# Kernel tuning notes

Measured on AMD Instinct MI355X. Metric: run time of the kernel, lower is better.

The kernel has to match this reference:

```python
import jax, jax.numpy as jnp
import numpy as np

EMB = 768
HEADS = 12
DH = EMB // HEADS


def setup_inputs() -> dict:
    key = jax.random.key(0)
    k = jax.random.split(key, 5)
    s = 0.02
    return {
        "x": jax.random.normal(k[0], (4, 2048, EMB), dtype=jnp.float32),
        "qkv_w": jax.random.normal(k[1], (3 * EMB, EMB), dtype=jnp.float32) * s,  # torch Linear weight [out,in]
        "qkv_b": jax.random.normal(k[2], (3 * EMB,), dtype=jnp.float32) * s,
        "proj_w": jax.random.normal(k[3], (EMB, EMB), dtype=jnp.float32) * s,
        "proj_b": jax.random.normal(k[4], (EMB,), dtype=jnp.float32) * s,
    }


def reference(x, qkv_w, qkv_b, proj_w, proj_b):
    b, n, _ = x.shape
    qkv = x @ qkv_w.T + qkv_b  # [b, n, 3*EMB]
    # rearrange 'b n (h d qkv) -> qkv b h n d'
    qkv = qkv.reshape(b, n, HEADS, DH, 3)
    qkv = jnp.transpose(qkv, (4, 0, 2, 1, 3))  # [3, b, h, n, d]
    q, k, v = qkv[0], qkv[1], qkv[2]
    e = jnp.einsum("bhqd,bhkd->bhqk", q, k)
    scale = jnp.float32(EMB) ** 0.5
    # NOTE: original divides by sqrt(emb_size) AFTER softmax (faithful to source)
    attn = jax.nn.softmax(e, axis=-1) / scale
    out = jnp.einsum("bhqk,bhkd->bhqd", attn, v)
    out = jnp.transpose(out, (0, 2, 1, 3)).reshape(b, n, EMB)  # 'b h n d -> b n (h d)'
    return out @ proj_w.T + proj_b
```

## Files before the change

### kernel.cpp

```cpp
#include <hip/hip_runtime.h>
#include <hip/hip_bf16.h>

typedef unsigned short ushort_t;
typedef __attribute__((ext_vector_type(8))) short s16x8;
typedef __attribute__((ext_vector_type(4))) float f32x4;
typedef __attribute__((ext_vector_type(16))) float f32x16;
typedef __attribute__((ext_vector_type(4))) unsigned int u32x4;

#define EMB 768
#define HEADS 12
#define DH 64
#define BATCH 4
#define SEQ 2048
#define MTOK (BATCH*SEQ)
#define NQKV (3*EMB)
#define LOG2E 1.44269504088896f

__device__ __forceinline__ ushort_t f2bf(float f) {
  unsigned u = __float_as_uint(f);
  u += 0x7fffu + ((u >> 16) & 1u);
  return (ushort_t)(u >> 16);
}
__device__ __forceinline__ unsigned pk2bf(float a, float b) {
  return (unsigned)f2bf(a) | ((unsigned)f2bf(b) << 16);
}
__device__ __forceinline__ unsigned cvtpk(float lo, float hi_) {
  unsigned d;
  asm("v_cvt_pk_bf16_f32 %0, %1, %2" : "=v"(d) : "v"(lo), "v"(hi_));
  return d;
}

__device__ __forceinline__ void gload_lds16(const void* g, void* l) {
  __builtin_amdgcn_global_load_lds(
      (const __attribute__((address_space(1))) unsigned*)g,
      (__attribute__((address_space(3))) unsigned*)l, 16, 0, 0);
}

__global__ void cvt_bf16(const float* __restrict__ in, ushort_t* __restrict__ out, int n4) {
  int i = blockIdx.x * blockDim.x + threadIdx.x;
  if (i >= n4) return;
  const float4 v = reinterpret_cast<const float4*>(in)[i];
  reinterpret_cast<uint2*>(out)[i] = make_uint2(pk2bf(v.x, v.y), pk2bf(v.z, v.w));
}

__global__ void cvt_wqkv(const float* __restrict__ w, const float* __restrict__ bias,
                         ushort_t* __restrict__ out, float* __restrict__ bias_p, int n4) {
  int i = blockIdx.x * blockDim.x + threadIdx.x;
  if (i >= n4) return;
  const int srcrow = i / 192;
  const int c4 = i - srcrow * 192;
  const int h = srcrow / 192;
  const int rem = srcrow - h * 192;
  const int d = rem / 3;
  const int which = rem - d * 3;
  const int dstrow = which * 768 + h * 64 + d;
  const float4 v = reinterpret_cast<const float4*>(w)[i];
  reinterpret_cast<uint2*>(out)[dstrow * 192 + c4] =
      make_uint2(pk2bf(v.x, v.y), pk2bf(v.z, v.w));
  if (c4 == 0) bias_p[dstrow] = bias[srcrow];
}

#define TM 128
#define TN 128
#define BKG 64
#define GSTEPS 12

template<int MODE>
__global__ __launch_bounds__(256, 2) void gemm_bt(
    const ushort_t* __restrict__ A, const ushort_t* __restrict__ BT,
    const float* __restrict__ bias, float* __restrict__ Cf,
    ushort_t* __restrict__ Qd, ushort_t* __restrict__ Kd, ushort_t* __restrict__ Vt,
    int M, int N, int K)
{
  __shared__ alignas(16) ushort_t As[2][TM*BKG];
  __shared__ alignas(16) ushort_t Bs[2][TN*BKG];
  const int t = threadIdx.x;
  const int w = t >> 6, l = t & 63, g = l >> 4, r = l & 15;
  const int wr = w >> 1, wc = w & 1;
  int lin = blockIdx.y * gridDim.x + blockIdx.x;
  const int cpx = (gridDim.x * gridDim.y) >> 3;
  lin = (lin & 7) * cpx + (lin >> 3);
  const int m0 = (lin / gridDim.x) * TM, n0 = (lin - (lin / gridDim.x) * gridDim.x) * TN;

  f32x4 acc[4][4] = {};

#define GSTAGE(bufc, st)                                                           \
  {                                                                                \
    const int kt = (st) * BKG;                                                     \
    _Pragma("unroll")                                                              \
    for (int p = 0; p < 4; ++p) {                                                  \
      const int off = (t + p*256) * 16;                     \
      const int row = off >> 7;                                  \
      const int scb = (off & 127) ^ ((row & 7) << 4);                              \
      gload_lds16(A  + (size_t)(m0+row)*K + kt + (scb>>1), (char*)&As[bufc][0] + off); \
      gload_lds16(BT + (size_t)(n0+row)*K + kt + (scb>>1), (char*)&Bs[bufc][0] + off); \
    }                                                                              \
  }

#define GCOMP(bufc)                                                                \
  {                                                                                \
    s16x8 fa[4][2], fb[4][2];                                                      \
    _Pragma("unroll")                                                              \
    for (int mi = 0; mi < 4; ++mi)                                                 \
      _Pragma("unroll")                                                            \
      for (int kk = 0; kk < 2; ++kk) {                                             \
        const int ra = wr*64 + mi*16 + r;                                          \
        fa[mi][kk] = *(const s16x8*)((const char*)&As[bufc][0] + ra*128 +          \
                                     ((g*16 + kk*64) ^ ((ra&7)<<4)));              \
        const int rb = wc*64 + mi*16 + r;                                          \
        fb[mi][kk] = *(const s16x8*)((const char*)&Bs[bufc][0] + rb*128 +          \
                                     ((g*16 + kk*64) ^ ((rb&7)<<4)));              \
      }                                                                            \
    __builtin_amdgcn_s_setprio(1);                                                 \
    _Pragma("unroll")                                                              \
    for (int mi = 0; mi < 4; ++mi)                                                 \
      _Pragma("unroll")                                                            \
      for (int ni = 0; ni < 4; ++ni) {                                             \
        acc[mi][ni] = __builtin_amdgcn_mfma_f32_16x16x32_bf16(                     \
            fa[mi][0], fb[ni][0], acc[mi][ni], 0, 0, 0);                           \
        acc[mi][ni] = __builtin_amdgcn_mfma_f32_16x16x32_bf16(                     \
            fa[mi][1], fb[ni][1], acc[mi][ni], 0, 0, 0);                           \
      }                                                                            \
    __builtin_amdgcn_s_setprio(0);                                                 \
  }

#define GITER(cur, st)                                                             \
  {                                                                                \
    asm volatile("s_barrier" ::: "memory");                                        \
    { const int s1 = (st) + 1 < GSTEPS ? (st) + 1 : GSTEPS - 1;                    \
      GSTAGE((cur) ^ 1, s1); }                                                     \
    asm volatile("s_waitcnt vmcnt(8)" ::: "memory");                               \
    asm volatile("s_barrier" ::: "memory");                                        \
    GCOMP(cur);                                                                    \
  }

  GSTAGE(0, 0);
#pragma unroll
  for (int s = 0; s < GSTEPS; ++s) GITER(s & 1, s);
#undef GITER
#undef GCOMP
#undef GSTAGE

#pragma unroll
  for (int ni = 0; ni < 4; ++ni) {
    const int col = n0 + wc*64 + ni*16 + r;
    const float bv = bias[col];
    if (MODE == 0) {
#pragma unroll
      for (int mi = 0; mi < 4; ++mi)
#pragma unroll
        for (int q = 0; q < 4; ++q) {
          const int rowg = m0 + wr*64 + mi*16 + g*4 + q;
          Cf[(size_t)rowg * N + col] = acc[mi][ni][q] + bv;
        }
    } else {
      const int which = col / 768;
      const int h_ = (col - which * 768) >> 6;
      const int d_ = col & 63;
      if (which == 2) {
#pragma unroll
        for (int mi = 0; mi < 4; ++mi) {
          const int nn0 = m0 + wr*64 + mi*16 + g*4;
          const int bb = nn0 >> 11, nl = nn0 & 2047;
          const int np0 = (nl & ~12) | ((nl & 4) << 1) | ((nl & 8) >> 1);
          uint2 u;
          u.x = pk2bf(acc[mi][ni][0] + bv, acc[mi][ni][1] + bv);
          u.y = pk2bf(acc[mi][ni][2] + bv, acc[mi][ni][3] + bv);
          *reinterpret_cast<uint2*>(Vt + ((size_t)(bb*HEADS + h_)*DH + d_)*SEQ + np0) = u;
        }
      } else {
        ushort_t* dst = (which == 0) ? Qd : Kd;
        const float sc = (which == 0) ? LOG2E : 1.0f;
#pragma unroll
        for (int mi = 0; mi < 4; ++mi)
#pragma unroll
          for (int q = 0; q < 4; ++q) {
            const int rowg = m0 + wr*64 + mi*16 + g*4 + q;
            const int bb = rowg >> 11, nn = rowg & 2047;
            dst[((size_t)(bb*HEADS + h_)*SEQ + nn)*DH + d_] =
                f2bf((acc[mi][ni][q] + bv) * sc);
          }
      }
    }
  }
}

#define NTIL 32

__global__ __launch_bounds__(256, 3) void attn_fwd(
    const ushort_t* __restrict__ Qd, const ushort_t* __restrict__ Kd,
    const ushort_t* __restrict__ Vt, ushort_t* __restrict__ Oa)
{
  __shared__ alignas(16) char L[3][16384];
  char* Lc = &L[0][0];

  const int t = threadIdx.x;
  const int w = t >> 6, l = t & 63;
  const int c31 = l & 31, hi = l >> 5;
  const int blk = blockIdx.x;
  const int logical = (blk & 7) * 96 + (blk >> 3);
  const int bh = logical >> 4;
  const int qt = logical & 15;
  const int q0 = qt * 128 + w * 32;
  const int b = bh / HEADS, h = bh - b * HEADS;

  const ushort_t* Qp = Qd + (size_t)bh * SEQ * DH;
  const ushort_t* Kp = Kd + (size_t)bh * SEQ * DH;
  const ushort_t* Vp = Vt + (size_t)bh * DH * SEQ;

  s16x8 qf[4];
  {
    const ushort_t* qp = Qp + (size_t)(q0 + c31) * DH + hi * 8;
#pragma unroll
    for (int c = 0; c < 4; ++c) qf[c] = *(const s16x8*)(qp + c * 16);
  }

  f32x16 oacc0 = {}, oacc1 = {};
  float ps0 = 0.f, ps1 = 0.f, ps2 = 0.f, ps3 = 0.f;

  const int ldsb = hi * 1024 + c31 * 16;
  const ushort_t* ksrc0 = Kp + (size_t)l * DH + w * 16;
  const ushort_t* vsrc0 = Vp + (size_t)l * SEQ + w * 16;
  char* kdst0 = Lc + w * 2048 + l * 16;

#define STAGE(bufc, tile_)                                                         \
  {                                                                                \
    const int tl = (tile_);                                                        \
    const ushort_t* ks = ksrc0 + (size_t)tl * (64 * DH);                           \
    const ushort_t* vs = vsrc0 + tl * 64;                                          \
    char* kd = kdst0 + (bufc) * 16384;                                             \
    gload_lds16(ks,     kd);                                                       \
    gload_lds16(ks + 8, kd + 1024);                                                \
    gload_lds16(vs,     kd + 8192);                                                \
    gload_lds16(vs + 8, kd + 9216);                                                \
  }

#define KGROUP(bufc, kg)                                                           \
  {                                                                                \
    const char* base = Lc + (bufc) * 16384 + ldsb;                                 \
    s16x8 kf0 = *(const s16x8*)(base + ((kg)*512 + 0*2048));                       \
    s16x8 kf1 = *(const s16x8*)(base + ((kg)*512 + 1*2048));                       \
    s16x8 kf2 = *(const s16x8*)(base + ((kg)*512 + 2*2048));                       \
    s16x8 kf3 = *(const s16x8*)(base + ((kg)*512 + 3*2048));                       \
    s16x8 va00 = *(const s16x8*)(base + (8192 + (kg)*4096 + 0*2048 + 0*512));      \
    s16x8 va01 = *(const s16x8*)(base + (8192 + (kg)*4096 + 1*2048 + 0*512));      \
    s16x8 va10 = *(const s16x8*)(base + (8192 + (kg)*4096 + 0*2048 + 1*512));      \
    s16x8 va11 = *(const s16x8*)(base + (8192 + (kg)*4096 + 1*2048 + 1*512));      \
    __builtin_amdgcn_s_setprio(1);                                                 \
    f32x16 s = {};                                                                 \
    s = __builtin_amdgcn_mfma_f32_32x32x16_bf16(kf0, qf[0], s, 0, 0, 0);           \
    s = __builtin_amdgcn_mfma_f32_32x32x16_bf16(kf1, qf[1], s, 0, 0, 0);           \
    s = __builtin_amdgcn_mfma_f32_32x32x16_bf16(kf2, qf[2], s, 0, 0, 0);           \
    s = __builtin_amdgcn_mfma_f32_32x32x16_bf16(kf3, qf[3], s, 0, 0, 0);           \
    __builtin_amdgcn_s_setprio(0);                                                 \
    float pe[16];                                                                  \
    _Pragma("unroll")                                                              \
    for (int r2 = 0; r2 < 16; ++r2) pe[r2] = __builtin_amdgcn_exp2f(s[r2]);        \
    ps0 += (pe[0]  + pe[1])  + (pe[2]  + pe[3]);                                   \
    ps1 += (pe[4]  + pe[5])  + (pe[6]  + pe[7]);                                   \
    ps2 += (pe[8]  + pe[9])  + (pe[10] + pe[11]);                                  \
    ps3 += (pe[12] + pe[13]) + (pe[14] + pe[15]);                                  \
    u32x4 f0u = { cvtpk(pe[0],  pe[1]),  cvtpk(pe[2],  pe[3]),                     \
                  cvtpk(pe[4],  pe[5]),  cvtpk(pe[6],  pe[7]) };                   \
    u32x4 f1u = { cvtpk(pe[8],  pe[9]),  cvtpk(pe[10], pe[11]),                    \
                  cvtpk(pe[12], pe[13]), cvtpk(pe[14], pe[15]) };                  \
    const s16x8 pf0 = __builtin_bit_cast(s16x8, f0u);                              \
    const s16x8 pf1 = __builtin_bit_cast(s16x8, f1u);                              \
    __builtin_amdgcn_s_setprio(1);                                                 \
    oacc0 = __builtin_amdgcn_mfma_f32_32x32x16_bf16(va00, pf0, oacc0, 0, 0, 0);    \
    oacc0 = __builtin_amdgcn_mfma_f32_32x32x16_bf16(va01, pf1, oacc0, 0, 0, 0);    \
    oacc1 = __builtin_amdgcn_mfma_f32_32x32x16_bf16(va10, pf0, oacc1, 0, 0, 0);    \
    oacc1 = __builtin_amdgcn_mfma_f32_32x32x16_bf16(va11, pf1, oacc1, 0, 0, 0);    \
    __builtin_amdgcn_s_setprio(0);                                                 \
  }

#define ITER(bufcur, bufn2, tt)                                                    \
  {                                                                                \
    asm volatile("s_barrier" ::: "memory");                                        \
    const int nt2 = (tt) + 2 < NTIL ? (tt) + 2 : NTIL - 1;                         \
    STAGE(bufn2, nt2);                                                             \
    asm volatile("s_waitcnt vmcnt(8)" ::: "memory");                               \
    asm volatile("s_barrier" ::: "memory");                                        \
    KGROUP(bufcur, 0);                                                             \
    KGROUP(bufcur, 1);                                                             \
  }

  STAGE(0, 0);
  STAGE(1, 1);
  for (int tt = 0; tt < NTIL - 2; tt += 3) {
    ITER(0, 2, tt);
    ITER(1, 0, tt + 1);
    ITER(2, 1, tt + 2);
  }
  ITER(0, 2, 30);
  ITER(1, 0, 31);
#undef ITER
#undef KGROUP
#undef STAGE

  const float psum = (ps0 + ps1) + (ps2 + ps3);
  const float lt = psum + __shfl_xor(psum, 32);
  const float scale = 0.036084391824351615f / lt;

  ushort_t* op = Oa + ((size_t)(b * SEQ + q0 + c31)) * EMB + h * DH;
#pragma unroll
  for (int f = 0; f < 2; ++f) {
    const f32x16& o = f ? oacc1 : oacc0;
#pragma unroll
    for (int rq = 0; rq < 4; ++rq) {
      const int dbase = f * 32 + 8 * rq + 4 * hi;
      uint2 u;
      u.x = pk2bf(o[rq*4+0] * scale, o[rq*4+1] * scale);
      u.y = pk2bf(o[rq*4+2] * scale, o[rq*4+3] * scale);
      *reinterpret_cast<uint2*>(op + dbase) = u;
    }
  }
}

extern "C" void kernel_launch(void* const* d_in, const int* in_sizes, int n_in,
                              void* d_out, int out_size, void* d_ws, size_t ws_size,
                              hipStream_t stream) {
  const float* x      = (const float*)d_in[0];
  const float* qkv_w  = (const float*)d_in[1];
  const float* qkv_b  = (const float*)d_in[2];
  const float* proj_w = (const float*)d_in[3];
  const float* proj_b = (const float*)d_in[4];
  float* out = (float*)d_out;

  ushort_t* xb    = (ushort_t*)d_ws;
  ushort_t* wqkv  = xb    + (size_t)MTOK*EMB;
  ushort_t* wproj = wqkv  + (size_t)NQKV*EMB;
  ushort_t* Qd    = wproj + (size_t)EMB*EMB;
  ushort_t* Kd    = Qd    + (size_t)MTOK*EMB;
  ushort_t* Vt    = Kd    + (size_t)MTOK*EMB;
  ushort_t* Oa    = Vt    + (size_t)MTOK*EMB;
  float*    biasp = (float*)(Oa + (size_t)MTOK*EMB);

  {
    int n4 = MTOK*EMB/4;
    cvt_bf16<<<(n4+255)/256, 256, 0, stream>>>(x, xb, n4);
  }
  {
    int n4 = NQKV*EMB/4;
    cvt_wqkv<<<(n4+255)/256, 256, 0, stream>>>(qkv_w, qkv_b, wqkv, biasp, n4);
  }
  {
    int n4 = EMB*EMB/4;
    cvt_bf16<<<(n4+255)/256, 256, 0, stream>>>(proj_w, wproj, n4);
  }

  gemm_bt<1><<<dim3(NQKV/TN, MTOK/TM), 256, 0, stream>>>(
      xb, wqkv, biasp, nullptr, Qd, Kd, Vt, MTOK, NQKV, EMB);

  attn_fwd<<<768, 256, 0, stream>>>(Qd, Kd, Vt, Oa);

  gemm_bt<0><<<dim3(EMB/TN, MTOK/TM), 256, 0, stream>>>(
      Oa, wproj, proj_b, out, nullptr, nullptr, nullptr, MTOK, EMB, EMB);
}
```

Measured before the change: 146.0 us.

## Split attention over two KV halves with a separate combine kernel

Splits each query tile's key range into two halves, so attention runs as 1536 blocks instead of 768. Each block writes an unnormalized partial output and its row sum, and a new combine kernel adds the two halves, normalizes and writes the heads-interleaved layout. LDS drops from triple to double buffering so occupancy can rise to 5 blocks per CU. In exchange it adds a kernel launch, extra global traffic for the partial outputs, and rounds the partials to bf16 before they are summed. This relies on the softmax having no max subtraction, so the halves combine by plain addition.

```diff
diff --git a/kernel.cpp b/kernel.cpp
--- a/kernel.cpp
+++ b/kernel.cpp
@@ -14,6 +14,7 @@
 #define SEQ 2048
 #define MTOK (BATCH*SEQ)
 #define NQKV (3*EMB)
+#define NBH (BATCH*HEADS)
 #define LOG2E 1.44269504088896f
 
 __device__ __forceinline__ ushort_t f2bf(float f) {
@@ -185,24 +186,27 @@
   }
 }
 
-#define NTIL 32
-
-__global__ __launch_bounds__(256, 3) void attn_fwd(
+#define NTILH 16
+
+__global__ __launch_bounds__(256, 5) void attn_fwd(
     const ushort_t* __restrict__ Qd, const ushort_t* __restrict__ Kd,
-    const ushort_t* __restrict__ Vt, ushort_t* __restrict__ Oa)
+    const ushort_t* __restrict__ Vt, ushort_t* __restrict__ Op0,
+    ushort_t* __restrict__ Op1, float* __restrict__ Lp)
 {
-  __shared__ alignas(16) char L[3][16384];
+  __shared__ alignas(16) char L[2][16384];
   char* Lc = &L[0][0];
 
   const int t = threadIdx.x;
   const int w = t >> 6, l = t & 63;
   const int c31 = l & 31, hi = l >> 5;
   const int blk = blockIdx.x;
-  const int logical = (blk & 7) * 96 + (blk >> 3);
-  const int bh = logical >> 4;
-  const int qt = logical & 15;
+  const int logical = (blk & 7) * 192 + (blk >> 3);
+  const int bh = logical >> 5;
+  const int rem = logical & 31;
+  const int half = rem >> 4;
+  const int qt = rem & 15;
   const int q0 = qt * 128 + w * 32;
-  const int b = bh / HEADS, h = bh - b * HEADS;
+  const int tb = half * NTILH;
 
   const ushort_t* Qp = Qd + (size_t)bh * SEQ * DH;
   const ushort_t* Kp = Kd + (size_t)bh * SEQ * DH;
@@ -274,35 +278,31 @@
     __builtin_amdgcn_s_setprio(0);                                                 \
   }
 
-#define ITER(bufcur, bufn2, tt)                                                    \
+#define ITER(cur, tt)                                                              \
   {                                                                                \
     asm volatile("s_barrier" ::: "memory");                                        \
-    const int nt2 = (tt) + 2 < NTIL ? (tt) + 2 : NTIL - 1;                         \
-    STAGE(bufn2, nt2);                                                             \
-    asm volatile("s_waitcnt vmcnt(8)" ::: "memory");                               \
+    { const int n1 = (tt) + 1 < NTILH ? (tt) + 1 : NTILH - 1;                      \
+      STAGE((cur) ^ 1, tb + n1); }                                                 \
+    asm volatile("s_waitcnt vmcnt(4)" ::: "memory");                               \
     asm volatile("s_barrier" ::: "memory");                                        \
-    KGROUP(bufcur, 0);                                                             \
-    KGROUP(bufcur, 1);                                                             \
-  }
-
-  STAGE(0, 0);
-  STAGE(1, 1);
-  for (int tt = 0; tt < NTIL - 2; tt += 3) {
-    ITER(0, 2, tt);
-    ITER(1, 0, tt + 1);
-    ITER(2, 1, tt + 2);
-  }
-  ITER(0, 2, 30);
-  ITER(1, 0, 31);
+    KGROUP(cur, 0);                                                                \
+    KGROUP(cur, 1);                                                                \
+  }
+
+  STAGE(0, tb);
+  for (int tt = 0; tt < NTILH; tt += 2) {
+    ITER(0, tt);
+    ITER(1, tt + 1);
+  }
 #undef ITER
 #undef KGROUP
 #undef STAGE
 
   const float psum = (ps0 + ps1) + (ps2 + ps3);
   const float lt = psum + __shfl_xor(psum, 32);
-  const float scale = 0.036084391824351615f / lt;
-
-  ushort_t* op = Oa + ((size_t)(b * SEQ + q0 + c31)) * EMB + h * DH;
+
+  ushort_t* Op = half ? Op1 : Op0;
+  ushort_t* op = Op + ((size_t)bh * SEQ + q0 + c31) * DH;
 #pragma unroll
   for (int f = 0; f < 2; ++f) {
     const f32x16& o = f ? oacc1 : oacc0;
@@ -310,11 +310,38 @@
     for (int rq = 0; rq < 4; ++rq) {
       const int dbase = f * 32 + 8 * rq + 4 * hi;
       uint2 u;
-      u.x = pk2bf(o[rq*4+0] * scale, o[rq*4+1] * scale);
-      u.y = pk2bf(o[rq*4+2] * scale, o[rq*4+3] * scale);
+      u.x = pk2bf(o[rq*4+0], o[rq*4+1]);
+      u.y = pk2bf(o[rq*4+2], o[rq*4+3]);
       *reinterpret_cast<uint2*>(op + dbase) = u;
     }
   }
+  if (l < 32)
+    Lp[(size_t)half * (NBH * SEQ) + (size_t)bh * SEQ + q0 + c31] = lt;
+}
+
+__global__ void attn_combine(const ushort_t* __restrict__ Op0,
+                             const ushort_t* __restrict__ Op1,
+                             const float* __restrict__ Lp,
+                             ushort_t* __restrict__ Oa) {
+  const int i = blockIdx.x * blockDim.x + threadIdx.x;
+  const int dseg = (i & 7) * 8;
+  const int n = (i >> 3) & (SEQ - 1);
+  const int bh = i >> 14;
+  const int b = bh / HEADS, h = bh - b * HEADS;
+  const size_t src = ((size_t)bh * SEQ + n) * DH + dseg;
+  const u32x4 a = *reinterpret_cast<const u32x4*>(Op0 + src);
+  const u32x4 c = *reinterpret_cast<const u32x4*>(Op1 + src);
+  const float lsum = Lp[(size_t)bh * SEQ + n] + Lp[(size_t)NBH * SEQ + (size_t)bh * SEQ + n];
+  const float s = 0.036084391824351615f / lsum;
+  u32x4 rr;
+#pragma unroll
+  for (int j = 0; j < 4; ++j) {
+    const unsigned x = a[j], y = c[j];
+    const float x0 = __uint_as_float(x << 16), x1 = __uint_as_float(x & 0xffff0000u);
+    const float y0 = __uint_as_float(y << 16), y1 = __uint_as_float(y & 0xffff0000u);
+    rr[j] = pk2bf((x0 + y0) * s, (x1 + y1) * s);
+  }
+  *reinterpret_cast<u32x4*>(Oa + ((size_t)(b * SEQ + n) * EMB + h * DH + dseg)) = rr;
 }
 
 extern "C" void kernel_launch(void* const* d_in, const int* in_sizes, int n_in,
@@ -335,6 +362,9 @@
   ushort_t* Vt    = Kd    + (size_t)MTOK*EMB;
   ushort_t* Oa    = Vt    + (size_t)MTOK*EMB;
   float*    biasp = (float*)(Oa + (size_t)MTOK*EMB);
+  ushort_t* Op1   = (ushort_t*)(biasp + 4096);
+  float*    Lp    = (float*)(Op1 + (size_t)MTOK*EMB);
+  ushort_t* Op0   = xb;
 
   {
     int n4 = MTOK*EMB/4;
@@ -352,7 +382,9 @@
   gemm_bt<1><<<dim3(NQKV/TN, MTOK/TM), 256, 0, stream>>>(
       xb, wqkv, biasp, nullptr, Qd, Kd, Vt, MTOK, NQKV, EMB);
 
-  attn_fwd<<<768, 256, 0, stream>>>(Qd, Kd, Vt, Oa);
+  attn_fwd<<<1536, 256, 0, stream>>>(Qd, Kd, Vt, Op0, Op1, Lp);
+
+  attn_combine<<<(NBH*SEQ*8)/256, 256, 0, stream>>>(Op0, Op1, Lp, Oa);
 
   gemm_bt<0><<<dim3(EMB/TN, MTOK/TM), 256, 0, stream>>>(
       Oa, wproj, proj_b, out, nullptr, nullptr, nullptr, MTOK, EMB, EMB);
```

Result: slower. 385.9 us (+164.3%).
